# Kernel tuning notes

Measured on AMD Instinct MI355X. Metric: run time of the kernel, lower is better.

The kernel has to match this reference:

```python
import jax, jax.numpy as jnp
import numpy as np

N = 10000        # nodes
E = 160000       # edges (before self-loops)
NFEAT = 256
NHID = 128
H = 4            # heads
NCLASS = 40
NLAYERS = 2
DT = 1.0
ALPHA = 1.0
GAMMA = 1.0
NEG_SLOPE = 0.2  # GATConv leaky_relu slope


def setup_inputs() -> dict:
    key = jax.random.key(0)
    ks = jax.random.split(key, 12)

    def glorot(k, shape):
        fan_in, fan_out = shape[-1], shape[0]
        lim = (6.0 / (fan_in + fan_out)) ** 0.5
        return jax.random.uniform(k, shape, jnp.float32, -lim, lim)

    return {
        "x": jax.random.normal(ks[0], (N, NFEAT), jnp.float32),
        "edge_index": jax.random.randint(ks[1], (2, E), 0, N, jnp.int64),
        "enc_w": glorot(ks[2], (NHID, NFEAT)),
        "enc_b": jnp.zeros((NHID,), jnp.float32),
        "res_w": glorot(ks[3], (H * NHID, NHID)),
        "res_b": jnp.zeros((H * NHID,), jnp.float32),
        "gat_w": glorot(ks[4], (H * NHID, NHID)),
        "att_src": glorot(ks[5], (H, NHID)) * 0.1,
        "att_dst": glorot(ks[6], (H, NHID)) * 0.1,
        "gat_b": jnp.zeros((H * NHID,), jnp.float32),
        "dec_w": glorot(ks[7], (NCLASS, NHID)),
        "dec_b": jnp.zeros((NCLASS,), jnp.float32),
    }


def _gat_conv(x, src, dst, gat_w, att_src, att_dst, gat_b):
    # x: [N, NHID] -> per-head features [N, H, C]
    xh = (x @ gat_w.T).reshape(N, H, NHID)
    a_src = jnp.sum(xh * att_src[None], axis=-1)  # [N, H]
    a_dst = jnp.sum(xh * att_dst[None], axis=-1)  # [N, H]
    e = jax.nn.leaky_relu(a_src[src] + a_dst[dst], NEG_SLOPE)  # [E', H]
    # segment softmax over incoming edges of each destination node
    m = jax.ops.segment_max(e, dst, num_segments=N)            # [N, H]
    e = jnp.exp(e - m[dst])
    s = jax.ops.segment_sum(e, dst, num_segments=N)            # [N, H]
    alpha = e / s[dst]                                          # [E', H]
    msg = xh[src] * alpha[:, :, None]                           # [E', H, C]
    out = jax.ops.segment_sum(msg, dst, num_segments=N)         # [N, H, C]
    return out.reshape(N, H * NHID) + gat_b


def reference(x, edge_index, enc_w, enc_b, res_w, res_b, gat_w,
              att_src, att_dst, gat_b, dec_w, dec_b):
    # add self-loops (GATConv default)
    loop = jnp.arange(N, dtype=edge_index.dtype)
    src = jnp.concatenate([edge_index[0], loop])
    dst = jnp.concatenate([edge_index[1], loop])

    Y = jax.nn.relu(x @ enc_w.T + enc_b)  # [N, NHID]
    X = Y
    for _ in range(NLAYERS):
        conv = _gat_conv(X, src, dst, gat_w, att_src, att_dst, gat_b)  # [N, H*NHID]
        res = X @ res_w.T + res_b                                       # [N, H*NHID]
        # faithful to .view(n_nodes, -1, nheads).mean(-1): [N, NHID, H] -> mean over heads axis
        z = jax.nn.elu(conv + res).reshape(N, NHID, H).mean(axis=-1)    # [N, NHID]
        Y = Y + DT * (z - ALPHA * Y - GAMMA * X)
        X = X + DT * Y
    return X @ dec_w.T + dec_b  # [N, NCLASS]
```

## Files before the change

### kernel.cpp

```cpp
#include <hip/hip_runtime.h>
#include <math.h>

#define NN 10000
#define EE 160000
#define EP 170000
#define NFEAT 256
#define NHID 128
#define NH 4
#define HF 512
#define NCLASS 40
#define FCOLS 1088

typedef __attribute__((ext_vector_type(8))) short bf8;
typedef __attribute__((ext_vector_type(8))) unsigned short u16x8;
typedef __attribute__((ext_vector_type(4))) float f4;

__device__ __forceinline__ float leaky02(float x) { return x >= 0.0f ? x : 0.2f * x; }

__device__ __forceinline__ unsigned short f2bf(float f) {
    unsigned u = __builtin_bit_cast(unsigned, f);
    unsigned r = (u + 0x7FFF + ((u >> 16) & 1)) >> 16;
    return (unsigned short)r;
}
__device__ __forceinline__ float bf2f(unsigned short h) {
    return __builtin_bit_cast(float, (unsigned)h << 16);
}

__device__ __forceinline__ int swz(int row, int c) {
    return ((((c >> 3) ^ (row & 7)) << 3) | (c & 7));
}

__device__ __forceinline__ void gl_lds16(const unsigned short* g, unsigned short* l)
{
    __builtin_amdgcn_global_load_lds(
        (const __attribute__((address_space(1))) unsigned int*)g,
        (__attribute__((address_space(3))) unsigned int*)l, 16, 0, 0);
}

__global__ __launch_bounds__(256)
void count_edges_k(const int* __restrict__ ei, int* __restrict__ cnt)
{
    int e = blockIdx.x * 256 + threadIdx.x;
    if (e >= EP) return;
    int d = (e < EE) ? ei[EE + e] : (e - EE);
    atomicAdd(&cnt[d], 1);
}

__global__ __launch_bounds__(1024)
void scan_k(const int* __restrict__ cnt, int* __restrict__ row_ptr)
{
    __shared__ int sm[1024];
    int t = threadIdx.x;
    int i0 = t * 10, i1 = min(i0 + 10, NN);
    int part = 0;
    for (int i = i0; i < i1; ++i) part += cnt[i];
    sm[t] = part;
    __syncthreads();
    for (int off = 1; off < 1024; off <<= 1) {
        int v = (t >= off) ? sm[t - off] : 0;
        __syncthreads();
        sm[t] += v;
        __syncthreads();
    }
    int run = sm[t] - part;
    for (int i = i0; i < i1; ++i) { row_ptr[i] = run; run += cnt[i]; }
    if (t == 1023) row_ptr[NN] = run;
}

__global__ __launch_bounds__(256)
void fill_csr_k(const int* __restrict__ ei, const int* __restrict__ row_ptr,
                int* __restrict__ cursor, int* __restrict__ csr)
{
    int e = blockIdx.x * 256 + threadIdx.x;
    if (e >= EP) return;
    int s, d;
    if (e < EE) { s = ei[e]; d = ei[EE + e]; } else { s = e - EE; d = s; }
    int pos = row_ptr[d] + atomicAdd(&cursor[d], 1);
    csr[pos] = s;
}

#define C_X   2560000
#define C_EW  (C_X + 32768)
#define C_FW  (C_EW + 131072)
#define C_DW  (C_FW + 5120)

__global__ __launch_bounds__(256)
void cvt_all_k(const float* __restrict__ x, const float* __restrict__ enc_w,
               const float* __restrict__ gat_w, const float* __restrict__ res_w,
               const float* __restrict__ dec_w,
               unsigned short* __restrict__ xhi, unsigned short* __restrict__ xlo,
               unsigned short* __restrict__ ewhi, unsigned short* __restrict__ ewlo,
               unsigned short* __restrict__ fwhi, unsigned short* __restrict__ fwlo,
               unsigned short* __restrict__ dwhi, unsigned short* __restrict__ dwlo)
{
    int iu = blockIdx.x * 256 + threadIdx.x;
    int i = iu * 8;
    if (i >= C_DW) return;
    const float* src = nullptr; unsigned short *ph, *pl; int j, row, c, Kd;
    if (i < C_X)       { j = i;        src = x;     ph = xhi;  pl = xlo;
                         row = j >> 8; c = j & 255; Kd = 256; }
    else if (i < C_EW) { j = i - C_X;  src = enc_w; ph = ewhi; pl = ewlo;
                         row = j >> 8; c = j & 255; Kd = 256; }
    else if (i < C_FW) { j = i - C_EW; ph = fwhi;   pl = fwlo;
                         row = j >> 7; c = j & 127; Kd = 128; }
    else               { j = i - C_FW; src = dec_w; ph = dwhi; pl = dwlo;
                         row = j >> 7; c = j & 127; Kd = 128; }

    float4 v0, v1;
    if (src) { v0 = *(const float4*)(src + j); v1 = *(const float4*)(src + j + 4); }
    else {
        const float* s2 = (j < 65536) ? (gat_w + j) : (res_w + j - 65536);
        v0 = *(const float4*)s2; v1 = *(const float4*)(s2 + 4);
    }
    float vv[8] = {v0.x, v0.y, v0.z, v0.w, v1.x, v1.y, v1.z, v1.w};
    unsigned short hs[8], ls[8];
#pragma unroll
    for (int k = 0; k < 8; ++k) {
        hs[k] = f2bf(vv[k]);
        ls[k] = f2bf(vv[k] - bf2f(hs[k]));
    }
    int out = row * Kd + swz(row, c);
    *(u16x8*)(ph + out) = *(u16x8*)hs;
    *(u16x8*)(pl + out) = *(u16x8*)ls;
}

__global__ __launch_bounds__(256)
void attw_k(const float* __restrict__ gat_w, const float* __restrict__ att_src,
            const float* __restrict__ att_dst,
            unsigned short* __restrict__ fwhi, unsigned short* __restrict__ fwlo)
{
    __shared__ float sm[256];
    int b = blockIdx.x;
    int is_dst = b >> 2, h = b & 3;
    const float* att = is_dst ? att_dst : att_src;
    int t = threadIdx.x;
    int k = t & 127, half = t >> 7;
    float s = 0.0f;
#pragma unroll 4
    for (int c = half * 64; c < half * 64 + 64; ++c)
        s = fmaf(gat_w[(size_t)(h * 128 + c) * 128 + k], att[h * 128 + c], s);
    sm[t] = s;
    __syncthreads();
    if (t < 128) {
        float v = sm[t] + sm[t + 128];
        int R = 1024 + is_dst * 4 + h;
        size_t o = (size_t)R * 128 + swz(R, k);
        unsigned short hi = f2bf(v);
        fwhi[o] = hi;
        fwlo[o] = f2bf(v - bf2f(hi));
    }
    for (int i = b * 896 + t; i < (b + 1) * 896; i += 256) {
        fwhi[1032 * 128 + i] = 0;
        fwlo[1032 * 128 + i] = 0;
    }
}

template<int MODE, int KTILES>
__global__ __launch_bounds__(256)
void gemm3_k(const unsigned short* __restrict__ Ahi, const unsigned short* __restrict__ Alo,
             const unsigned short* __restrict__ Bhi, const unsigned short* __restrict__ Blo,
             const float* __restrict__ bias,
             float* __restrict__ outF, unsigned short* __restrict__ outH,
             unsigned short* __restrict__ outL,
             float* __restrict__ a_src, float* __restrict__ a_dst, int M)
{
    constexpr int K = KTILES * 128;
    __shared__ __align__(16) unsigned short smem[4 * 64 * 128];
    unsigned short* sAh = smem;
    unsigned short* sAl = smem + 8192;
    unsigned short* sBh = smem + 16384;
    unsigned short* sBl = smem + 24576;

    const int tid = threadIdx.x;
    const int lane = tid & 63, wv = tid >> 6;
    const int wr = (wv >> 1) * 32, wc = (wv & 1) * 32;
    const int bm = blockIdx.x * 64, bn = blockIdx.y * 64;
    const int r16 = lane & 15, q4 = lane >> 4;

    f4 acc[2][2];
#pragma unroll
    for (int i = 0; i < 2; ++i)
#pragma unroll
        for (int j = 0; j < 2; ++j) acc[i][j] = (f4){0.f, 0.f, 0.f, 0.f};

    const int ra0 = wr + r16;
    const int rb0 = wc + r16;

    for (int kt = 0; kt < KTILES; ++kt) {
        if (kt) __syncthreads();
#pragma unroll
        for (int j = 0; j < 4; ++j) {
            int i = tid + j * 256;
            int row = i >> 4, u = i & 15;
            int arow = min(bm + row, M - 1);
            int brow = bn + row;
            size_t ga = (size_t)arow * K + kt * 128 + u * 8;
            size_t gb = (size_t)brow * K + kt * 128 + u * 8;
            int lb = (wv * 64 + j * 256) * 8;
            gl_lds16(Ahi + ga, sAh + lb);
            gl_lds16(Alo + ga, sAl + lb);
            gl_lds16(Bhi + gb, sBh + lb);
            gl_lds16(Blo + gb, sBl + lb);
        }
        __syncthreads();

#pragma unroll
        for (int ks = 0; ks < 4; ++ks) {
            int u = ks * 4 + q4;
            int oa0 = ra0 * 128 + ((u ^ (ra0 & 7)) * 8);
            int ob0 = rb0 * 128 + ((u ^ (rb0 & 7)) * 8);
            int oa1 = oa0 + 16 * 128;
            int ob1 = ob0 + 16 * 128;
            bf8 A0h = *(const bf8*)(sAh + oa0);
            bf8 A1h = *(const bf8*)(sAh + oa1);
            bf8 A0l = *(const bf8*)(sAl + oa0);
            bf8 A1l = *(const bf8*)(sAl + oa1);
            bf8 B0h = *(const bf8*)(sBh + ob0);
            bf8 B1h = *(const bf8*)(sBh + ob1);
            bf8 B0l = *(const bf8*)(sBl + ob0);
            bf8 B1l = *(const bf8*)(sBl + ob1);

            acc[0][0] = __builtin_amdgcn_mfma_f32_16x16x32_bf16(A0h, B0h, acc[0][0], 0, 0, 0);
            acc[0][1] = __builtin_amdgcn_mfma_f32_16x16x32_bf16(A0h, B1h, acc[0][1], 0, 0, 0);
            acc[1][0] = __builtin_amdgcn_mfma_f32_16x16x32_bf16(A1h, B0h, acc[1][0], 0, 0, 0);
            acc[1][1] = __builtin_amdgcn_mfma_f32_16x16x32_bf16(A1h, B1h, acc[1][1], 0, 0, 0);
            acc[0][0] = __builtin_amdgcn_mfma_f32_16x16x32_bf16(A0h, B0l, acc[0][0], 0, 0, 0);
            acc[0][1] = __builtin_amdgcn_mfma_f32_16x16x32_bf16(A0h, B1l, acc[0][1], 0, 0, 0);
            acc[1][0] = __builtin_amdgcn_mfma_f32_16x16x32_bf16(A1h, B0l, acc[1][0], 0, 0, 0);
            acc[1][1] = __builtin_amdgcn_mfma_f32_16x16x32_bf16(A1h, B1l, acc[1][1], 0, 0, 0);
            acc[0][0] = __builtin_amdgcn_mfma_f32_16x16x32_bf16(A0l, B0h, acc[0][0], 0, 0, 0);
            acc[0][1] = __builtin_amdgcn_mfma_f32_16x16x32_bf16(A0l, B1h, acc[0][1], 0, 0, 0);
            acc[1][0] = __builtin_amdgcn_mfma_f32_16x16x32_bf16(A1l, B0h, acc[1][0], 0, 0, 0);
            acc[1][1] = __builtin_amdgcn_mfma_f32_16x16x32_bf16(A1l, B1h, acc[1][1], 0, 0, 0);
        }
    }

    const int rbase = q4 * 4;

    if (MODE == 0 || (MODE == 2 && bn >= 1024)) {
#pragma unroll
        for (int i = 0; i < 2; ++i)
#pragma unroll
            for (int j = 0; j < 2; ++j)
#pragma unroll
                for (int r = 0; r < 4; ++r) {
                    int row = bm + wr + i * 16 + rbase + r;
                    int col = bn + wc + j * 16 + r16;
                    if (row >= M) continue;
                    float v = acc[i][j][r];
                    if (MODE == 0) {
                        if (col < NCLASS)
                            outF[(size_t)row * NCLASS + col] = v + bias[col];
                    } else {
                        if (col < 1032) {
                            int h = col - 1024;
                            if (h < 4) a_src[row * 4 + h] = v;
                            else       a_dst[row * 4 + h - 4] = v;
                        }
                    }
                }
        return;
    }

    __syncthreads();
    float* sC = (float*)smem;
#pragma unroll
    for (int i = 0; i < 2; ++i)
#pragma unroll
        for (int j = 0; j < 2; ++j)
#pragma unroll
            for (int r = 0; r < 4; ++r)
                sC[(wr + i * 16 + rbase + r) * 65 + (wc + j * 16 + r16)] = acc[i][j][r];
    __syncthreads();

    int row = tid >> 2, seg = tid & 3, c0 = seg * 16;
    int grow = bm + row;
    if (grow >= M) return;
    float v[16];
#pragma unroll
    for (int k = 0; k < 16; ++k) v[k] = sC[row * 65 + c0 + k];

    if (MODE == 1) {
        unsigned short hs[16], ls[16];
#pragma unroll
        for (int k = 0; k < 16; ++k) {
            float u = fmaxf(v[k] + bias[bn + c0 + k], 0.0f);
            hs[k] = f2bf(u);
            ls[k] = f2bf(u - bf2f(hs[k]));
        }
#pragma unroll
        for (int uu = 0; uu < 2; ++uu) {
            int ug = (bn + c0) / 8 + uu;
            int pu = ug ^ (grow & 7);
            *(u16x8*)(outH + (size_t)grow * 128 + pu * 8) = *(u16x8*)(hs + uu * 8);
            *(u16x8*)(outL + (size_t)grow * 128 + pu * 8) = *(u16x8*)(ls + uu * 8);
        }
    } else {
        if (bn < 512) {
            unsigned short hs[16];
#pragma unroll
            for (int k = 0; k < 16; ++k) hs[k] = f2bf(v[k]);
            *(u16x8*)(outH + (size_t)grow * 512 + bn + c0)     = *(u16x8*)hs;
            *(u16x8*)(outH + (size_t)grow * 512 + bn + c0 + 8) = *(u16x8*)(hs + 8);
        } else {
#pragma unroll
            for (int k = 0; k < 16; ++k) v[k] += bias[bn - 512 + c0 + k];
            float* dst = outF + (size_t)grow * 512 + (bn - 512) + c0;
#pragma unroll
            for (int k4 = 0; k4 < 4; ++k4)
                *(float4*)(dst + k4 * 4) =
                    make_float4(v[k4 * 4], v[k4 * 4 + 1], v[k4 * 4 + 2], v[k4 * 4 + 3]);
        }
    }
}

__global__ __launch_bounds__(256)
void agg_k(const int* __restrict__ row_ptr, const int* __restrict__ csr,
           const float* __restrict__ a_src, const float* __restrict__ a_dst,
           const unsigned short* __restrict__ xh_b, const float* __restrict__ res,
           const float* __restrict__ gat_b,
           unsigned short* __restrict__ Xhi, unsigned short* __restrict__ Xlo)
{
    int wave = threadIdx.x >> 6, lane = threadIdx.x & 63;
    int d = blockIdx.x * 4 + wave;
    if (d >= NN) return;
    int beg = row_ptr[d], end = row_ptr[d + 1];
    int hl = lane >> 4;
    int cb = lane * 8;
    float ad = a_dst[d * 4 + hl];

    float acc[8];
#pragma unroll
    for (int k = 0; k < 8; ++k) acc[k] = 0.0f;
    float ssum = 0.0f;

    int e = beg;
    for (; e + 8 <= end; e += 8) {
        int sv[8]; float w[8]; u16x8 v[8];
#pragma unroll
        for (int q = 0; q < 8; ++q) sv[q] = csr[e + q];
#pragma unroll
        for (int q = 0; q < 8; ++q) v[q] = *(const u16x8*)(xh_b + (size_t)sv[q] * HF + cb);
#pragma unroll
        for (int q = 0; q < 8; ++q) {
            w[q] = __expf(leaky02(a_src[sv[q] * 4 + hl] + ad));
            ssum += w[q];
        }
#pragma unroll
        for (int q = 0; q < 8; ++q)
#pragma unroll
            for (int k = 0; k < 8; ++k) acc[k] = fmaf(w[q], bf2f(v[q][k]), acc[k]);
    }
    for (; e + 4 <= end; e += 4) {
        int sv[4]; float w[4]; u16x8 v[4];
#pragma unroll
        for (int q = 0; q < 4; ++q) sv[q] = csr[e + q];
#pragma unroll
        for (int q = 0; q < 4; ++q) v[q] = *(const u16x8*)(xh_b + (size_t)sv[q] * HF + cb);
#pragma unroll
        for (int q = 0; q < 4; ++q) {
            w[q] = __expf(leaky02(a_src[sv[q] * 4 + hl] + ad));
            ssum += w[q];
        }
#pragma unroll
        for (int q = 0; q < 4; ++q)
#pragma unroll
            for (int k = 0; k < 8; ++k) acc[k] = fmaf(w[q], bf2f(v[q][k]), acc[k]);
    }
    for (; e < end; ++e) {
        int s = csr[e];
        float w = __expf(leaky02(a_src[s * 4 + hl] + ad));
        ssum += w;
        u16x8 v = *(const u16x8*)(xh_b + (size_t)s * HF + cb);
#pragma unroll
        for (int k = 0; k < 8; ++k) acc[k] = fmaf(w, bf2f(v[k]), acc[k]);
    }

    float inv = 1.0f / ssum;
    const float* rr = res + (size_t)d * HF + cb;
    const float* gb = gat_b + cb;
    float u[8];
#pragma unroll
    for (int k = 0; k < 8; ++k) {
        float v = fmaf(acc[k], inv, gb[k] + rr[k]);
        u[k] = (v > 0.0f) ? v : expm1f(v);
    }
    float z0 = (u[0] + u[1] + u[2] + u[3]) * 0.25f;
    float z1 = (u[4] + u[5] + u[6] + u[7]) * 0.25f;
    unsigned short h0 = f2bf(z0), h1 = f2bf(z1);
    unsigned short l0 = f2bf(z0 - bf2f(h0)), l1 = f2bf(z1 - bf2f(h1));
    int pos = swz(d, lane * 2);
    size_t idx = (size_t)d * NHID + pos;
    *(unsigned*)(Xhi + idx) = ((unsigned)h1 << 16) | h0;
    *(unsigned*)(Xlo + idx) = ((unsigned)l1 << 16) | l0;
}

extern "C" void kernel_launch(void* const* d_in, const int* in_sizes, int n_in,
                              void* d_out, int out_size, void* d_ws, size_t ws_size,
                              hipStream_t stream)
{
    const float* x       = (const float*)d_in[0];
    const int*   ei      = (const int*)d_in[1];
    const float* enc_w   = (const float*)d_in[2];
    const float* enc_b   = (const float*)d_in[3];
    const float* res_w   = (const float*)d_in[4];
    const float* res_b   = (const float*)d_in[5];
    const float* gat_w   = (const float*)d_in[6];
    const float* att_src = (const float*)d_in[7];
    const float* att_dst = (const float*)d_in[8];
    const float* gat_b   = (const float*)d_in[9];
    const float* dec_w   = (const float*)d_in[10];
    const float* dec_b   = (const float*)d_in[11];
    float* out = (float*)d_out;

    char* p = (char*)d_ws;
    auto alloc = [&](size_t bytes) -> void* {
        void* r = (void*)p;
        p += (bytes + 255) & ~(size_t)255;
        return r;
    };
    float* res    = (float*)alloc(5120000 * 4);
    float* a_src  = (float*)alloc(40000 * 4);
    float* a_dst  = (float*)alloc(40000 * 4);
    unsigned short* xh_b = (unsigned short*)alloc(5120000 * 2);
    unsigned short* Xhi  = (unsigned short*)alloc(1280000 * 2);
    unsigned short* Xlo  = (unsigned short*)alloc(1280000 * 2);
    unsigned short* xhi  = (unsigned short*)alloc(2560000 * 2);
    unsigned short* xlo  = (unsigned short*)alloc(2560000 * 2);
    unsigned short* ewhi = (unsigned short*)alloc(32768 * 2);
    unsigned short* ewlo = (unsigned short*)alloc(32768 * 2);
    unsigned short* fwhi = (unsigned short*)alloc(FCOLS * 128 * 2);
    unsigned short* fwlo = (unsigned short*)alloc(FCOLS * 128 * 2);
    int* row_ptr = (int*)alloc(10004 * 4);
    int* csr     = (int*)alloc(170000 * 4);
    char* zbase = p;
    unsigned short* dwhi = (unsigned short*)alloc(8192 * 2);
    unsigned short* dwlo = (unsigned short*)alloc(8192 * 2);
    int* cnt    = (int*)alloc(10000 * 4);
    int* cursor = (int*)alloc(10000 * 4);
    size_t zbytes = (size_t)(p - zbase);

    hipMemsetAsync(zbase, 0, zbytes, stream);

    int eb = (EP + 255) / 256;
    count_edges_k<<<eb, 256, 0, stream>>>(ei, cnt);
    scan_k<<<1, 1024, 0, stream>>>(cnt, row_ptr);
    fill_csr_k<<<eb, 256, 0, stream>>>(ei, row_ptr, cursor, csr);

    cvt_all_k<<<(C_DW / 8 + 255) / 256, 256, 0, stream>>>(
        x, enc_w, gat_w, res_w, dec_w,
        xhi, xlo, ewhi, ewlo, fwhi, fwlo, dwhi, dwlo);
    attw_k<<<8, 256, 0, stream>>>(gat_w, att_src, att_dst, fwhi, fwlo);

    gemm3_k<1, 2><<<dim3(157, 2), 256, 0, stream>>>(
        xhi, xlo, ewhi, ewlo, enc_b, nullptr, Xhi, Xlo, nullptr, nullptr, NN);

    for (int layer = 0; layer < 2; ++layer) {
        gemm3_k<2, 1><<<dim3(157, 17), 256, 0, stream>>>(
            Xhi, Xlo, fwhi, fwlo, res_b, res, xh_b, nullptr, a_src, a_dst, NN);
        agg_k<<<2500, 256, 0, stream>>>(row_ptr, csr, a_src, a_dst, xh_b, res, gat_b, Xhi, Xlo);
    }

    gemm3_k<0, 1><<<dim3(157, 1), 256, 0, stream>>>(
        Xhi, Xlo, dwhi, dwlo, dec_b, out, nullptr, nullptr, nullptr, nullptr, NN);
}
```

Baseline: 252.9 us.

## Fuse prep kernels, merge CSR build into GEMMs, store residual in bf16, split aggregation

Several changes land at once. Conversion, attention-weight folding, bias precombination and edge counting now run in one launch. The scan and CSR fill are folded into extra grid rows of the encoder and first GAT GEMMs. The residual projection is stored as bf16 with the combined res+gat bias instead of fp32, and the aggregation splits each destination's edge list across two waves that are reduced through shared memory. The aim is fewer launches, less residual traffic and more parallelism in aggregation, at the cost of bf16 rounding of the residual and an extra block sync.

```diff
diff --git a/kernel.cpp b/kernel.cpp
--- a/kernel.cpp
+++ b/kernel.cpp
@@ -37,141 +37,143 @@
         (__attribute__((address_space(3))) unsigned int*)l, 16, 0, 0);
 }
 
-__global__ __launch_bounds__(256)
-void count_edges_k(const int* __restrict__ ei, int* __restrict__ cnt)
-{
-    int e = blockIdx.x * 256 + threadIdx.x;
-    if (e >= EP) return;
-    int d = (e < EE) ? ei[EE + e] : (e - EE);
-    atomicAdd(&cnt[d], 1);
-}
-
-__global__ __launch_bounds__(1024)
-void scan_k(const int* __restrict__ cnt, int* __restrict__ row_ptr)
-{
-    __shared__ int sm[1024];
-    int t = threadIdx.x;
-    int i0 = t * 10, i1 = min(i0 + 10, NN);
-    int part = 0;
-    for (int i = i0; i < i1; ++i) part += cnt[i];
-    sm[t] = part;
-    __syncthreads();
-    for (int off = 1; off < 1024; off <<= 1) {
-        int v = (t >= off) ? sm[t - off] : 0;
-        __syncthreads();
-        sm[t] += v;
-        __syncthreads();
-    }
-    int run = sm[t] - part;
-    for (int i = i0; i < i1; ++i) { row_ptr[i] = run; run += cnt[i]; }
-    if (t == 1023) row_ptr[NN] = run;
-}
-
-__global__ __launch_bounds__(256)
-void fill_csr_k(const int* __restrict__ ei, const int* __restrict__ row_ptr,
-                int* __restrict__ cursor, int* __restrict__ csr)
-{
-    int e = blockIdx.x * 256 + threadIdx.x;
-    if (e >= EP) return;
-    int s, d;
-    if (e < EE) { s = ei[e]; d = ei[EE + e]; } else { s = e - EE; d = s; }
-    int pos = row_ptr[d] + atomicAdd(&cursor[d], 1);
-    csr[pos] = s;
-}
-
 #define C_X   2560000
 #define C_EW  (C_X + 32768)
 #define C_FW  (C_EW + 131072)
 #define C_DW  (C_FW + 5120)
+#define CVT_B  1333
+#define ATTW_B (CVT_B + 8)
+#define TOT_B  (ATTW_B + 166)
 
 __global__ __launch_bounds__(256)
-void cvt_all_k(const float* __restrict__ x, const float* __restrict__ enc_w,
-               const float* __restrict__ gat_w, const float* __restrict__ res_w,
-               const float* __restrict__ dec_w,
-               unsigned short* __restrict__ xhi, unsigned short* __restrict__ xlo,
-               unsigned short* __restrict__ ewhi, unsigned short* __restrict__ ewlo,
-               unsigned short* __restrict__ fwhi, unsigned short* __restrict__ fwlo,
-               unsigned short* __restrict__ dwhi, unsigned short* __restrict__ dwlo)
+void fused0_k(const float* __restrict__ x, const float* __restrict__ enc_w,
+              const float* __restrict__ gat_w, const float* __restrict__ res_w,
+              const float* __restrict__ dec_w, const float* __restrict__ att_src,
+              const float* __restrict__ att_dst, const float* __restrict__ res_b,
+              const float* __restrict__ gat_b, const int* __restrict__ ei,
+              unsigned short* __restrict__ xhi, unsigned short* __restrict__ xlo,
+              unsigned short* __restrict__ ewhi, unsigned short* __restrict__ ewlo,
+              unsigned short* __restrict__ fwhi, unsigned short* __restrict__ fwlo,
+              unsigned short* __restrict__ dwhi, unsigned short* __restrict__ dwlo,
+              float* __restrict__ biasRG, int* __restrict__ cnt)
 {
-    int iu = blockIdx.x * 256 + threadIdx.x;
-    int i = iu * 8;
-    if (i >= C_DW) return;
-    const float* src = nullptr; unsigned short *ph, *pl; int j, row, c, Kd;
-    if (i < C_X)       { j = i;        src = x;     ph = xhi;  pl = xlo;
-                         row = j >> 8; c = j & 255; Kd = 256; }
-    else if (i < C_EW) { j = i - C_X;  src = enc_w; ph = ewhi; pl = ewlo;
-                         row = j >> 8; c = j & 255; Kd = 256; }
-    else if (i < C_FW) { j = i - C_EW; ph = fwhi;   pl = fwlo;
-                         row = j >> 7; c = j & 127; Kd = 128; }
-    else               { j = i - C_FW; src = dec_w; ph = dwhi; pl = dwlo;
-                         row = j >> 7; c = j & 127; Kd = 128; }
-
-    float4 v0, v1;
-    if (src) { v0 = *(const float4*)(src + j); v1 = *(const float4*)(src + j + 4); }
-    else {
-        const float* s2 = (j < 65536) ? (gat_w + j) : (res_w + j - 65536);
-        v0 = *(const float4*)s2; v1 = *(const float4*)(s2 + 4);
-    }
-    float vv[8] = {v0.x, v0.y, v0.z, v0.w, v1.x, v1.y, v1.z, v1.w};
-    unsigned short hs[8], ls[8];
-#pragma unroll
-    for (int k = 0; k < 8; ++k) {
-        hs[k] = f2bf(vv[k]);
-        ls[k] = f2bf(vv[k] - bf2f(hs[k]));
-    }
-    int out = row * Kd + swz(row, c);
-    *(u16x8*)(ph + out) = *(u16x8*)hs;
-    *(u16x8*)(pl + out) = *(u16x8*)ls;
-}
-
-__global__ __launch_bounds__(256)
-void attw_k(const float* __restrict__ gat_w, const float* __restrict__ att_src,
-            const float* __restrict__ att_dst,
-            unsigned short* __restrict__ fwhi, unsigned short* __restrict__ fwlo)
-{
-    __shared__ float sm[256];
-    int b = blockIdx.x;
-    int is_dst = b >> 2, h = b & 3;
-    const float* att = is_dst ? att_dst : att_src;
+    int bId = blockIdx.x;
     int t = threadIdx.x;
-    int k = t & 127, half = t >> 7;
-    float s = 0.0f;
+    if (bId < CVT_B) {
+        int iu = bId * 256 + t;
+        int i = iu * 8;
+        if (i >= C_DW) return;
+        const float* src = nullptr; unsigned short *ph, *pl; int j, row, c, Kd;
+        if (i < C_X)       { j = i;        src = x;     ph = xhi;  pl = xlo;
+                             row = j >> 8; c = j & 255; Kd = 256; }
+        else if (i < C_EW) { j = i - C_X;  src = enc_w; ph = ewhi; pl = ewlo;
+                             row = j >> 8; c = j & 255; Kd = 256; }
+        else if (i < C_FW) { j = i - C_EW; ph = fwhi;   pl = fwlo;
+                             row = j >> 7; c = j & 127; Kd = 128; }
+        else               { j = i - C_FW; src = dec_w; ph = dwhi; pl = dwlo;
+                             row = j >> 7; c = j & 127; Kd = 128; }
+        float4 v0, v1;
+        if (src) { v0 = *(const float4*)(src + j); v1 = *(const float4*)(src + j + 4); }
+        else {
+            const float* s2 = (j < 65536) ? (gat_w + j) : (res_w + j - 65536);
+            v0 = *(const float4*)s2; v1 = *(const float4*)(s2 + 4);
+        }
+        float vv[8] = {v0.x, v0.y, v0.z, v0.w, v1.x, v1.y, v1.z, v1.w};
+        unsigned short hs[8], ls[8];
+#pragma unroll
+        for (int k = 0; k < 8; ++k) {
+            hs[k] = f2bf(vv[k]);
+            ls[k] = f2bf(vv[k] - bf2f(hs[k]));
+        }
+        int outp = row * Kd + swz(row, c);
+        *(u16x8*)(ph + outp) = *(u16x8*)hs;
+        *(u16x8*)(pl + outp) = *(u16x8*)ls;
+    } else if (bId < ATTW_B) {
+        __shared__ float sm[256];
+        int b = bId - CVT_B;
+        int is_dst = b >> 2, h = b & 3;
+        const float* att = is_dst ? att_dst : att_src;
+        int k = t & 127, half = t >> 7;
+        float s = 0.0f;
 #pragma unroll 4
-    for (int c = half * 64; c < half * 64 + 64; ++c)
-        s = fmaf(gat_w[(size_t)(h * 128 + c) * 128 + k], att[h * 128 + c], s);
-    sm[t] = s;
-    __syncthreads();
-    if (t < 128) {
-        float v = sm[t] + sm[t + 128];
-        int R = 1024 + is_dst * 4 + h;
-        size_t o = (size_t)R * 128 + swz(R, k);
-        unsigned short hi = f2bf(v);
-        fwhi[o] = hi;
-        fwlo[o] = f2bf(v - bf2f(hi));
-    }
-    for (int i = b * 896 + t; i < (b + 1) * 896; i += 256) {
-        fwhi[1032 * 128 + i] = 0;
-        fwlo[1032 * 128 + i] = 0;
-    }
-}
-
-template<int MODE, int KTILES>
+        for (int c = half * 64; c < half * 64 + 64; ++c)
+            s = fmaf(gat_w[(size_t)(h * 128 + c) * 128 + k], att[h * 128 + c], s);
+        sm[t] = s;
+        __syncthreads();
+        if (t < 128) {
+            float v = sm[t] + sm[t + 128];
+            int R = 1024 + is_dst * 4 + h;
+            size_t o = (size_t)R * 128 + swz(R, k);
+            unsigned short hi = f2bf(v);
+            fwhi[o] = hi;
+            fwlo[o] = f2bf(v - bf2f(hi));
+        }
+        for (int i = b * 896 + t; i < (b + 1) * 896; i += 256) {
+            fwhi[1032 * 128 + i] = 0;
+            fwlo[1032 * 128 + i] = 0;
+        }
+        if (b < 2) {
+            int c = b * 256 + t;
+            biasRG[c] = res_b[c] + gat_b[c];
+        }
+    } else {
+        for (int e = (bId - ATTW_B) * 256 + t; e < EP; e += (TOT_B - ATTW_B) * 256) {
+            int d = (e < EE) ? ei[EE + e] : (e - EE);
+            atomicAdd(&cnt[d], 1);
+        }
+    }
+}
+
+template<int MODE, int KTILES, int MERGE>
 __global__ __launch_bounds__(256)
 void gemm3_k(const unsigned short* __restrict__ Ahi, const unsigned short* __restrict__ Alo,
              const unsigned short* __restrict__ Bhi, const unsigned short* __restrict__ Blo,
              const float* __restrict__ bias,
              float* __restrict__ outF, unsigned short* __restrict__ outH,
              unsigned short* __restrict__ outL,
-             float* __restrict__ a_src, float* __restrict__ a_dst, int M)
+             float* __restrict__ a_src, float* __restrict__ a_dst, int M,
+             const int* __restrict__ ei, const int* __restrict__ cnt,
+             int* __restrict__ row_ptr, int* __restrict__ cursor, int* __restrict__ csr)
 {
     constexpr int K = KTILES * 128;
     __shared__ __align__(16) unsigned short smem[4 * 64 * 128];
+    const int tid = threadIdx.x;
+
+    if (MERGE && blockIdx.y == gridDim.y - 1) {
+        if (MERGE == 1) {
+            if (blockIdx.x != 0) return;
+            int* smi = (int*)smem;
+            int i0 = tid * 40, i1 = min(i0 + 40, NN);
+            int part = 0;
+            for (int i = i0; i < i1; ++i) part += cnt[i];
+            smi[tid] = part;
+            __syncthreads();
+            for (int off = 1; off < 256; off <<= 1) {
+                int v = (tid >= off) ? smi[tid - off] : 0;
+                __syncthreads();
+                smi[tid] += v;
+                __syncthreads();
+            }
+            int run = smi[tid] - part;
+            for (int i = i0; i < i1; ++i) { row_ptr[i] = run; run += cnt[i]; }
+            if (tid == 255) row_ptr[NN] = run;
+        } else {
+            int stride = gridDim.x * 256;
+            for (int e = blockIdx.x * 256 + tid; e < EP; e += stride) {
+                int s, d;
+                if (e < EE) { s = ei[e]; d = ei[EE + e]; } else { s = e - EE; d = s; }
+                int pos = row_ptr[d] + atomicAdd(&cursor[d], 1);
+                csr[pos] = s;
+            }
+        }
+        return;
+    }
+
     unsigned short* sAh = smem;
     unsigned short* sAl = smem + 8192;
     unsigned short* sBh = smem + 16384;
     unsigned short* sBl = smem + 24576;
 
-    const int tid = threadIdx.x;
     const int lane = tid & 63, wv = tid >> 6;
     const int wr = (wv >> 1) * 32, wc = (wv & 1) * 32;
     const int bm = blockIdx.x * 64, bn = blockIdx.y * 64;
@@ -303,13 +305,11 @@
             *(u16x8*)(outH + (size_t)grow * 512 + bn + c0)     = *(u16x8*)hs;
             *(u16x8*)(outH + (size_t)grow * 512 + bn + c0 + 8) = *(u16x8*)(hs + 8);
         } else {
-#pragma unroll
-            for (int k = 0; k < 16; ++k) v[k] += bias[bn - 512 + c0 + k];
-            float* dst = outF + (size_t)grow * 512 + (bn - 512) + c0;
-#pragma unroll
-            for (int k4 = 0; k4 < 4; ++k4)
-                *(float4*)(dst + k4 * 4) =
-                    make_float4(v[k4 * 4], v[k4 * 4 + 1], v[k4 * 4 + 2], v[k4 * 4 + 3]);
+            unsigned short hs[16];
+#pragma unroll
+            for (int k = 0; k < 16; ++k) hs[k] = f2bf(v[k] + bias[bn - 512 + c0 + k]);
+            *(u16x8*)(outL + (size_t)grow * 512 + (bn - 512) + c0)     = *(u16x8*)hs;
+            *(u16x8*)(outL + (size_t)grow * 512 + (bn - 512) + c0 + 8) = *(u16x8*)(hs + 8);
         }
     }
 }
@@ -317,25 +317,31 @@
 __global__ __launch_bounds__(256)
 void agg_k(const int* __restrict__ row_ptr, const int* __restrict__ csr,
            const float* __restrict__ a_src, const float* __restrict__ a_dst,
-           const unsigned short* __restrict__ xh_b, const float* __restrict__ res,
-           const float* __restrict__ gat_b,
+           const unsigned short* __restrict__ xh_b, const unsigned short* __restrict__ resb,
            unsigned short* __restrict__ Xhi, unsigned short* __restrict__ Xlo)
 {
-    int wave = threadIdx.x >> 6, lane = threadIdx.x & 63;
-    int d = blockIdx.x * 4 + wave;
-    if (d >= NN) return;
+    __shared__ float sAcc[2][64][8];
+    __shared__ float sSum[2][64];
+    int wv = threadIdx.x >> 6, lane = threadIdx.x & 63;
+    int pair = wv >> 1, half = wv & 1;
+    int d = blockIdx.x * 2 + pair;
     int beg = row_ptr[d], end = row_ptr[d + 1];
+    int len = end - beg;
+    int h0 = (len + 1) >> 1;
+    int eb = half ? (beg + h0) : beg;
+    int en = half ? end : (beg + h0);
     int hl = lane >> 4;
     int cb = lane * 8;
     float ad = a_dst[d * 4 + hl];
+    u16x8 rv = *(const u16x8*)(resb + (size_t)d * HF + cb);
 
     float acc[8];
 #pragma unroll
     for (int k = 0; k < 8; ++k) acc[k] = 0.0f;
     float ssum = 0.0f;
 
-    int e = beg;
-    for (; e + 8 <= end; e += 8) {
+    int e = eb;
+    for (; e + 8 <= en; e += 8) {
         int sv[8]; float w[8]; u16x8 v[8];
 #pragma unroll
         for (int q = 0; q < 8; ++q) sv[q] = csr[e + q];
@@ -351,7 +357,7 @@
 #pragma unroll
             for (int k = 0; k < 8; ++k) acc[k] = fmaf(w[q], bf2f(v[q][k]), acc[k]);
     }
-    for (; e + 4 <= end; e += 4) {
+    for (; e + 4 <= en; e += 4) {
         int sv[4]; float w[4]; u16x8 v[4];
 #pragma unroll
         for (int q = 0; q < 4; ++q) sv[q] = csr[e + q];
@@ -367,7 +373,7 @@
 #pragma unroll
             for (int k = 0; k < 8; ++k) acc[k] = fmaf(w[q], bf2f(v[q][k]), acc[k]);
     }
-    for (; e < end; ++e) {
+    for (; e < en; ++e) {
         int s = csr[e];
         float w = __expf(leaky02(a_src[s * 4 + hl] + ad));
         ssum += w;
@@ -376,23 +382,32 @@
         for (int k = 0; k < 8; ++k) acc[k] = fmaf(w, bf2f(v[k]), acc[k]);
     }
 
+    if (half) {
+        *(float4*)&sAcc[pair][lane][0] = make_float4(acc[0], acc[1], acc[2], acc[3]);
+        *(float4*)&sAcc[pair][lane][4] = make_float4(acc[4], acc[5], acc[6], acc[7]);
+        sSum[pair][lane] = ssum;
+    }
+    __syncthreads();
+    if (half) return;
+#pragma unroll
+    for (int k = 0; k < 8; ++k) acc[k] += sAcc[pair][lane][k];
+    ssum += sSum[pair][lane];
+
     float inv = 1.0f / ssum;
-    const float* rr = res + (size_t)d * HF + cb;
-    const float* gb = gat_b + cb;
     float u[8];
 #pragma unroll
     for (int k = 0; k < 8; ++k) {
-        float v = fmaf(acc[k], inv, gb[k] + rr[k]);
+        float v = fmaf(acc[k], inv, bf2f(rv[k]));
         u[k] = (v > 0.0f) ? v : expm1f(v);
     }
     float z0 = (u[0] + u[1] + u[2] + u[3]) * 0.25f;
     float z1 = (u[4] + u[5] + u[6] + u[7]) * 0.25f;
-    unsigned short h0 = f2bf(z0), h1 = f2bf(z1);
-    unsigned short l0 = f2bf(z0 - bf2f(h0)), l1 = f2bf(z1 - bf2f(h1));
+    unsigned short h0b = f2bf(z0), h1b = f2bf(z1);
+    unsigned short l0b = f2bf(z0 - bf2f(h0b)), l1b = f2bf(z1 - bf2f(h1b));
     int pos = swz(d, lane * 2);
     size_t idx = (size_t)d * NHID + pos;
-    *(unsigned*)(Xhi + idx) = ((unsigned)h1 << 16) | h0;
-    *(unsigned*)(Xlo + idx) = ((unsigned)l1 << 16) | l0;
+    *(unsigned*)(Xhi + idx) = ((unsigned)h1b << 16) | h0b;
+    *(unsigned*)(Xlo + idx) = ((unsigned)l1b << 16) | l0b;
 }
 
 extern "C" void kernel_launch(void* const* d_in, const int* in_sizes, int n_in,
@@ -419,10 +434,11 @@
         p += (bytes + 255) & ~(size_t)255;
         return r;
     };
-    float* res    = (float*)alloc(5120000 * 4);
     float* a_src  = (float*)alloc(40000 * 4);
     float* a_dst  = (float*)alloc(40000 * 4);
+    float* biasRG = (float*)alloc(512 * 4);
     unsigned short* xh_b = (unsigned short*)alloc(5120000 * 2);
+    unsigned short* resb = (unsigned short*)alloc(5120000 * 2);
     unsigned short* Xhi  = (unsigned short*)alloc(1280000 * 2);
     unsigned short* Xlo  = (unsigned short*)alloc(1280000 * 2);
     unsigned short* xhi  = (unsigned short*)alloc(2560000 * 2);
@@ -442,25 +458,25 @@
 
     hipMemsetAsync(zbase, 0, zbytes, stream);
 
-    int eb = (EP + 255) / 256;
-    count_edges_k<<<eb, 256, 0, stream>>>(ei, cnt);
-    scan_k<<<1, 1024, 0, stream>>>(cnt, row_ptr);
-    fill_csr_k<<<eb, 256, 0, stream>>>(ei, row_ptr, cursor, csr);
-
-    cvt_all_k<<<(C_DW / 8 + 255) / 256, 256, 0, stream>>>(
-        x, enc_w, gat_w, res_w, dec_w,
-        xhi, xlo, ewhi, ewlo, fwhi, fwlo, dwhi, dwlo);
-    attw_k<<<8, 256, 0, stream>>>(gat_w, att_src, att_dst, fwhi, fwlo);
-
-    gemm3_k<1, 2><<<dim3(157, 2), 256, 0, stream>>>(
-        xhi, xlo, ewhi, ewlo, enc_b, nullptr, Xhi, Xlo, nullptr, nullptr, NN);
-
-    for (int layer = 0; layer < 2; ++layer) {
-        gemm3_k<2, 1><<<dim3(157, 17), 256, 0, stream>>>(
-            Xhi, Xlo, fwhi, fwlo, res_b, res, xh_b, nullptr, a_src, a_dst, NN);
-        agg_k<<<2500, 256, 0, stream>>>(row_ptr, csr, a_src, a_dst, xh_b, res, gat_b, Xhi, Xlo);
-    }
-
-    gemm3_k<0, 1><<<dim3(157, 1), 256, 0, stream>>>(
-        Xhi, Xlo, dwhi, dwlo, dec_b, out, nullptr, nullptr, nullptr, nullptr, NN);
-}
+    fused0_k<<<TOT_B, 256, 0, stream>>>(
+        x, enc_w, gat_w, res_w, dec_w, att_src, att_dst, res_b, gat_b, ei,
+        xhi, xlo, ewhi, ewlo, fwhi, fwlo, dwhi, dwlo, biasRG, cnt);
+
+    gemm3_k<1, 2, 1><<<dim3(157, 3), 256, 0, stream>>>(
+        xhi, xlo, ewhi, ewlo, enc_b, nullptr, Xhi, Xlo, nullptr, nullptr, NN,
+        nullptr, cnt, row_ptr, nullptr, nullptr);
+
+    gemm3_k<2, 1, 2><<<dim3(157, 18), 256, 0, stream>>>(
+        Xhi, Xlo, fwhi, fwlo, biasRG, nullptr, xh_b, resb, a_src, a_dst, NN,
+        ei, nullptr, row_ptr, cursor, csr);
+    agg_k<<<5000, 256, 0, stream>>>(row_ptr, csr, a_src, a_dst, xh_b, resb, Xhi, Xlo);
+
+    gemm3_k<2, 1, 0><<<dim3(157, 17), 256, 0, stream>>>(
+        Xhi, Xlo, fwhi, fwlo, biasRG, nullptr, xh_b, resb, a_src, a_dst, NN,
+        nullptr, nullptr, nullptr, nullptr, nullptr);
+    agg_k<<<5000, 256, 0, stream>>>(row_ptr, csr, a_src, a_dst, xh_b, resb, Xhi, Xlo);
+
+    gemm3_k<0, 1, 0><<<dim3(157, 1), 256, 0, stream>>>(
+        Xhi, Xlo, dwhi, dwlo, dec_b, out, nullptr, nullptr, nullptr, nullptr, NN,
+        nullptr, nullptr, nullptr, nullptr, nullptr);
+}
```

New measurement: 225.2 us. -11.0%, faster.
